# Kernel tuning notes

Hardware: AMD Instinct MI355X
Metric: run time of the kernel (lower is better)

The kernel has to match this reference:

```python
import jax, jax.numpy as jnp
import numpy as np


def _elem_mlp(x, w1, b1, w2, b2):
    # elementwise 1 -> N -> 1 ReLU MLP (distilled exp / inv approximators)
    h = jax.nn.relu(x[..., None] * w1[:, 0] + b1)  # [..., N]
    return jnp.einsum('...n,n->...', h, w2[0]) + b2[0]


def setup_inputs() -> dict:
    key = jax.random.key(0)
    ks = jax.random.split(key, 13)
    T, S, B, D = 8, 512, 8, 512
    NE, NI = 32, 64
    f = jnp.float32
    inp = {
        'sx': jax.random.normal(ks[0], (T, S, B, D), f) * 0.1,
        'q_proj_weight': jax.random.normal(ks[1], (D, D), f) / np.sqrt(D),
        'k_proj_weight': jax.random.normal(ks[2], (D, D), f) / np.sqrt(D),
        'q_proj_bias': jax.random.normal(ks[3], (D,), f) * 0.02,
        'k_proj_bias': jax.random.normal(ks[4], (D,), f) * 0.02,
        'exp_w1': jax.random.normal(ks[5], (NE, 1), f),
        'exp_b1': jax.random.normal(ks[6], (NE,), f) * 0.1,
        'exp_w2': jax.random.normal(ks[7], (1, NE), f) / np.sqrt(NE),
        'exp_b2': jax.random.normal(ks[8], (1,), f) * 0.01,
        'inv_w1': jax.random.normal(ks[9], (NI, 1), f),
        'inv_b1': jax.random.normal(ks[10], (NI,), f) * 0.1,
        'inv_w2': jax.random.normal(ks[11], (1, NI), f) / np.sqrt(NI),
        'inv_b2': jax.random.normal(ks[12], (1,), f) * 0.01,
        'num_heads': 8,
    }
    return inp


def reference(sx, q_proj_weight, k_proj_weight, q_proj_bias, k_proj_bias,
              exp_w1, exp_b1, exp_w2, exp_b2,
              inv_w1, inv_b1, inv_w2, inv_b2, num_heads):
    T, S, B, D = sx.shape
    H = num_heads
    hd = D // H
    scale = 1.0 / np.sqrt(hd)

    def proj(x_t, W, b):
        # [S, B, D] -> [B*H, S, hd]
        y = x_t @ W.T + b
        return y.reshape(S, B * H, hd).transpose(1, 0, 2)

    def step(carry, x_t):
        sum_q, sum_k, sum_p = carry
        sq = proj(x_t, q_proj_weight, q_proj_bias)
        sk = proj(x_t, k_proj_weight, k_proj_bias)
        sum_q = sum_q + sq
        # sp_t = sum_q @ sk^T + sq @ sum_k^T (sum_k updated AFTER, per snn_qk_product)
        sp = (jnp.einsum('bsh,bth->bst', sum_q, sk)
              + jnp.einsum('bsh,bth->bst', sq, sum_k)) * scale
        sum_k = sum_k + sk
        return (sum_q, sum_k, sum_p + sp), None

    z_qk = jnp.zeros((B * H, S, hd), sx.dtype)
    z_p = jnp.zeros((B * H, S, S), sx.dtype)
    (sum_q, sum_k, sum_p), _ = jax.lax.scan(step, (z_qk, z_qk, z_p), sx)

    p = sum_p / T  # time-averaged accumulated QK product

    # fit_softmax: distilled-MLP softmax approximation
    tmax = p[:, :, 0:1]
    tp = jnp.minimum(p - (tmax - 1.0), 3.0)
    x_up = jnp.where(tp > -20.0,
                     _elem_mlp(tp, exp_w1, exp_b1, exp_w2, exp_b2), 0.0)
    partition = x_up.sum(-1, keepdims=True)
    p_inv = _elem_mlp(partition, inv_w1, inv_b1, inv_w2, inv_b2)
    out = x_up * p_inv
    partition_p2 = out.sum(-1, keepdims=True)
    p_inv2 = _elem_mlp(partition_p2, inv_w1, inv_b1, inv_w2, inv_b2)
    out2 = jnp.where(partition_p2 > 1.5, out * p_inv2, out)
    return out2
```

## Files before the change

### kernel.cpp

```cpp
#include <hip/hip_runtime.h>


#define T_  8
#define NE_ 32
#define NI_ 64

#define LUT_N   4096
#define LUT_LO  -20.0f
#define LUT_HI  3.0f
#define LUT_INVW (LUT_N / (LUT_HI - LUT_LO))
#define LUT_W    ((LUT_HI - LUT_LO) / LUT_N)

typedef __attribute__((ext_vector_type(8))) short bf16x8;
typedef __attribute__((ext_vector_type(4))) float f32x4;

#define XS_OFF 0u
#define WQ_OFF 2097152u
#define WK_OFF 2359296u
#define QB_OFF 2621440u
#define KB_OFF 4718592u
#define LUT_OFF 6815744u

__device__ inline unsigned short f2bf(float f) {
  union { float f; unsigned u; } v; v.f = f;
  unsigned r = v.u + 0x7FFFu + ((v.u >> 16) & 1u);
  return (unsigned short)(r >> 16);
}

__device__ inline void gload16(const void* g, void* l) {
  __builtin_amdgcn_global_load_lds(
      (const __attribute__((address_space(1))) void*)g,
      (__attribute__((address_space(3))) void*)l, 16, 0, 0);
}

__device__ inline bf16x8 lds_read_swz(const unsigned short* base, int row, int byteoff) {
  int addr = row * 128 + (byteoff ^ ((row & 7) << 4));
  return *(const bf16x8*)((const char*)base + addr);
}

__device__ inline float invmlp(float x, const float* __restrict__ w1,
                               const float* __restrict__ b1,
                               const float* __restrict__ w2, float b2) {
  float a = b2;
  for (int n = 0; n < NI_; n++) a += w2[n] * fmaxf(x * w1[n] + b1[n], 0.0f);
  return a;
}

__device__ inline float expmlp_exact(float t, const float* __restrict__ w1,
                                     const float* __restrict__ b1,
                                     const float* __restrict__ w2, float b2) {
  float a = b2;
#pragma unroll
  for (int n = 0; n < NE_; n++) a += w2[n] * fmaxf(t * w1[n] + b1[n], 0.0f);
  return a;
}

__global__ __launch_bounds__(256) void k_pre(
    const float* __restrict__ sx, const float* __restrict__ wq,
    const float* __restrict__ wk, const float* __restrict__ ew1,
    const float* __restrict__ eb1, const float* __restrict__ ew2,
    const float* __restrict__ eb2p,
    unsigned short* __restrict__ xs, unsigned short* __restrict__ wqb,
    unsigned short* __restrict__ wkb, float2* __restrict__ lut) {
  int bx = blockIdx.x, tid = threadIdx.x;
  if (bx < 2048) {
    size_t i = ((size_t)bx * 256 + tid) * 4;
    float4 a = *(const float4*)(sx + i);
#pragma unroll
    for (int t = 1; t < T_; t++) {
      float4 v = *(const float4*)(sx + (size_t)t * 2097152 + i);
      a.x += v.x; a.y += v.y; a.z += v.z; a.w += v.w;
    }
    ushort4 o; o.x = f2bf(a.x); o.y = f2bf(a.y); o.z = f2bf(a.z); o.w = f2bf(a.w);
    *(ushort4*)(xs + i) = o;
  } else if (bx < 2560) {
    const float* src = (bx < 2304) ? wq : wk;
    unsigned short* dst = (bx < 2304) ? wqb : wkb;
    int base = (bx < 2304) ? 2048 : 2304;
    size_t i = ((size_t)(bx - base) * 256 + tid) * 4;
    float4 a = *(const float4*)(src + i);
    ushort4 o; o.x = f2bf(a.x); o.y = f2bf(a.y); o.z = f2bf(a.z); o.w = f2bf(a.w);
    *(ushort4*)(dst + i) = o;
  } else {
    int i = (bx - 2560) * 256 + tid;
    float b2 = eb2p[0];
    float tl = fmaf((float)i, LUT_W, LUT_LO);
    float th = fmaf((float)(i + 1), LUT_W, LUT_LO);
    float el = expmlp_exact(tl, ew1, eb1, ew2, b2);
    float eh = expmlp_exact(th, ew1, eb1, ew2, b2);
    float alpha = (eh - el) * LUT_INVW;
    float beta = fmaf(-alpha, tl, el);
    lut[i] = make_float2(alpha, beta);
  }
}

__global__ __launch_bounds__(256, 2) void k_proj(
    const unsigned short* __restrict__ xs, const unsigned short* __restrict__ wb,
    const float* __restrict__ bq, const float* __restrict__ bk,
    unsigned short* __restrict__ outb) {
  __shared__ unsigned short As[128 * 64];
  __shared__ unsigned short Bs[128 * 64];
  int tid = threadIdx.x;
  int lane = tid & 63, w = tid >> 6;
  int r0 = blockIdx.x * 128;
  int c0 = blockIdx.y * 128;
  int z = blockIdx.z;
  const unsigned short* W = wb + (size_t)z * 262144;
  const float* bias = z ? bk : bq;
  unsigned short* dst = outb + (size_t)z * 2097152;
  float sc = z ? 1.0f : (1.0f / 64.0f);

  int rgrp = lane >> 4, cl = lane & 15;
  int r0w = (w >> 1) * 64, c0w = (w & 1) * 64;

  f32x4 acc[4][4];
  f32x4 zero = {0.f, 0.f, 0.f, 0.f};
#pragma unroll
  for (int m = 0; m < 4; m++)
#pragma unroll
    for (int n = 0; n < 4; n++) acc[m][n] = zero;

  int rl = lane >> 3, slot = lane & 7;

  for (int kt = 0; kt < 8; kt++) {
    int k0 = kt * 64;
#pragma unroll
    for (int i = 0; i < 4; i++) {
      int chunk = w * 4 + i;
      int r = chunk * 8 + rl;
      int sw = (slot ^ (r & 7)) * 8;
      gload16(xs + (size_t)(r0 + r) * 512 + k0 + sw, (char*)As + chunk * 1024);
      gload16(W + (size_t)(c0 + r) * 512 + k0 + sw, (char*)Bs + chunk * 1024);
    }
    __syncthreads();
#pragma unroll
    for (int kb = 0; kb < 2; kb++) {
      bf16x8 af[4], bfr[4];
#pragma unroll
      for (int m = 0; m < 4; m++) af[m] = lds_read_swz(As, r0w + 16 * m + cl, kb * 64 + rgrp * 16);
#pragma unroll
      for (int n = 0; n < 4; n++) bfr[n] = lds_read_swz(Bs, c0w + 16 * n + cl, kb * 64 + rgrp * 16);
#pragma unroll
      for (int m = 0; m < 4; m++)
#pragma unroll
        for (int n = 0; n < 4; n++)
          acc[m][n] = __builtin_amdgcn_mfma_f32_16x16x32_bf16(af[m], bfr[n], acc[m][n], 0, 0, 0);
    }
    __syncthreads();
  }

#pragma unroll
  for (int n = 0; n < 4; n++) {
    int cg = c0 + c0w + 16 * n + cl;
    float bv = 8.0f * bias[cg];
    int h = cg >> 6, dh = cg & 63;
#pragma unroll
    for (int m = 0; m < 4; m++) {
#pragma unroll
      for (int j = 0; j < 4; j++) {
        int rg = r0 + r0w + 16 * m + rgrp * 4 + j;
        int s = rg >> 3, b = rg & 7;
        dst[((size_t)(b * 8 + h) * 512 + s) * 64 + dh] = f2bf((acc[m][n][j] + bv) * sc);
      }
    }
  }
}

__global__ __launch_bounds__(512, 4) void k_attn(
    const unsigned short* __restrict__ qb, const unsigned short* __restrict__ kb,
    const float2* __restrict__ lutg,
    const float* __restrict__ iw1, const float* __restrict__ ib1,
    const float* __restrict__ iw2, const float* __restrict__ ib2p,
    float* __restrict__ out) {
  __shared__ float2 Lut[LUT_N];
  __shared__ float s_tmax[32];
  __shared__ float s_part[4][32];
  __shared__ float s_fac[32];

  int tid = threadIdx.x;
  int lane = tid & 63, w = tid >> 6;
  int rt = blockIdx.x, bh = blockIdx.y;
  int rs = w & 1, ch = w >> 1;
  int r0 = rt * 32;
  int c0 = ch * 128;
  int rgrp = lane >> 4, cl = lane & 15;

#pragma unroll
  for (int i = 0; i < 4; i++) {
    int chunk = w * 4 + i;
    gload16((const char*)lutg + chunk * 1024 + lane * 16, (char*)Lut + chunk * 1024);
  }

  const unsigned short* Kg = kb + (size_t)bh * (512 * 64);
  const unsigned short* Qg = qb + (size_t)bh * (512 * 64);

  const bf16x8* qrow = (const bf16x8*)(Qg + (size_t)(r0 + rs * 16 + cl) * 64);
  bf16x8 aF0 = qrow[rgrp];
  bf16x8 aF1 = qrow[4 + rgrp];

  f32x4 acc[8];
  f32x4 zero = {0.f, 0.f, 0.f, 0.f};
#pragma unroll
  for (int f = 0; f < 8; f++) {
    const bf16x8* krow = (const bf16x8*)(Kg + (size_t)(c0 + 16 * f + cl) * 64);
    bf16x8 b0 = krow[rgrp];
    bf16x8 b1 = krow[4 + rgrp];
    acc[f] = __builtin_amdgcn_mfma_f32_16x16x32_bf16(aF0, b0, zero, 0, 0, 0);
    acc[f] = __builtin_amdgcn_mfma_f32_16x16x32_bf16(aF1, b1, acc[f], 0, 0, 0);
  }

  if (ch == 0 && cl == 0) {
#pragma unroll
    for (int j = 0; j < 4; j++) s_tmax[rs * 16 + rgrp * 4 + j] = acc[0][j] - 1.0f;
  }
  __syncthreads();

  float tm1[4];
#pragma unroll
  for (int j = 0; j < 4; j++) tm1[j] = s_tmax[rs * 16 + rgrp * 4 + j];

  const float C0 = -LUT_LO * LUT_INVW;
  float rowsum[4] = {0.f, 0.f, 0.f, 0.f};
#pragma unroll
  for (int f = 0; f < 8; f++) {
#pragma unroll
    for (int j = 0; j < 4; j++) {
      float tp = fminf(acc[f][j] - tm1[j], 3.0f);
      float u = fmaf(tp, LUT_INVW, C0);
      u = fminf(fmaxf(u, 0.0f), (float)(LUT_N - 1));
      float2 ab = Lut[(int)u];
      float xu = fmaf(ab.x, tp, ab.y);
      xu = (tp > -20.0f) ? xu : 0.0f;
      acc[f][j] = xu;
      rowsum[j] += xu;
    }
  }

#pragma unroll
  for (int j = 0; j < 4; j++) {
    float s = rowsum[j];
    s += __shfl_xor(s, 1);
    s += __shfl_xor(s, 2);
    s += __shfl_xor(s, 4);
    s += __shfl_xor(s, 8);
    if (cl == 0) s_part[ch][rs * 16 + rgrp * 4 + j] = s;
  }
  __syncthreads();

  if (tid < 32) {
    float part = s_part[0][tid] + s_part[1][tid] + s_part[2][tid] + s_part[3][tid];
    float pinv = invmlp(part, iw1, ib1, iw2, ib2p[0]);
    float pp2 = part * pinv;
    float fac = pinv;
    if (pp2 > 1.5f) fac *= invmlp(pp2, iw1, ib1, iw2, ib2p[0]);
    s_fac[tid] = fac;
  }
  __syncthreads();

  float* outb = out + ((size_t)bh * 512 + r0) * 512;
#pragma unroll
  for (int j = 0; j < 4; j++) {
    int row = rs * 16 + rgrp * 4 + j;
    float fac = s_fac[row];
#pragma unroll
    for (int f = 0; f < 8; f++)
      outb[(size_t)row * 512 + c0 + 16 * f + cl] = acc[f][j] * fac;
  }
}

extern "C" void kernel_launch(void* const* d_in, const int* in_sizes, int n_in,
                              void* d_out, int out_size, void* d_ws, size_t ws_size,
                              hipStream_t stream) {
  (void)in_sizes; (void)n_in; (void)out_size; (void)ws_size;
  const float* sx  = (const float*)d_in[0];
  const float* wq  = (const float*)d_in[1];
  const float* wk  = (const float*)d_in[2];
  const float* bq  = (const float*)d_in[3];
  const float* bk  = (const float*)d_in[4];
  const float* ew1 = (const float*)d_in[5];
  const float* eb1 = (const float*)d_in[6];
  const float* ew2 = (const float*)d_in[7];
  const float* eb2 = (const float*)d_in[8];
  const float* iw1 = (const float*)d_in[9];
  const float* ib1 = (const float*)d_in[10];
  const float* iw2 = (const float*)d_in[11];
  const float* ib2 = (const float*)d_in[12];
  unsigned short* wsu = (unsigned short*)d_ws;
  float2* lut = (float2*)(wsu + LUT_OFF);
  float* out = (float*)d_out;

  k_pre<<<2576, 256, 0, stream>>>(sx, wq, wk, ew1, eb1, ew2, eb2,
                                  wsu + XS_OFF, wsu + WQ_OFF, wsu + WK_OFF, lut);
  k_proj<<<dim3(32, 4, 2), 256, 0, stream>>>(wsu + XS_OFF, wsu + WQ_OFF, bq, bk, wsu + QB_OFF);
  k_attn<<<dim3(16, 64), 512, 0, stream>>>(wsu + QB_OFF, wsu + KB_OFF, lut,
                                           iw1, ib1, iw2, ib2, out);
}
```

Measured before the change: 60.76 us.

## Pack Q/K in MFMA fragment layout and enlarge attention tiles with XCD-aware mapping

The projection kernel now writes Q and K in a fragment-packed layout, so each lane of the attention kernel loads its bf16x8 operand from one contiguous 16-byte slot. Before, each lane gathered strided pieces of 64-element rows. Each attention block now covers 64 rows by all 512 columns, with 16 accumulator fragments per wave. This halves the block count and the number of LUT copies loaded into LDS. Block indices are remapped so that blocks sharing a batch-head land on the same XCD for L2 reuse. The cost is higher register pressure from 16 live accumulators per wave, which may reduce occupancy.

```diff
diff --git a/kernel.cpp b/kernel.cpp
--- a/kernel.cpp
+++ b/kernel.cpp
@@ -154,13 +154,17 @@
     int cg = c0 + c0w + 16 * n + cl;
     float bv = 8.0f * bias[cg];
     int h = cg >> 6, dh = cg & 63;
+    int chunk = dh >> 3, hh = chunk >> 2, rg2 = chunk & 3, jj = dh & 7;
 #pragma unroll
     for (int m = 0; m < 4; m++) {
 #pragma unroll
       for (int j = 0; j < 4; j++) {
         int rg = r0 + r0w + 16 * m + rgrp * 4 + j;
         int s = rg >> 3, b = rg & 7;
-        dst[((size_t)(b * 8 + h) * 512 + s) * 64 + dh] = f2bf((acc[m][n][j] + bv) * sc);
+        int bh = b * 8 + h;
+        int cb = s >> 4, cls = s & 15;
+        size_t idx = ((size_t)((bh * 32 + cb) * 2 + hh)) * 512 + (rg2 * 16 + cls) * 8 + jj;
+        dst[idx] = f2bf((acc[m][n][j] + bv) * sc);
       }
     }
   }
@@ -173,38 +177,38 @@
     const float* __restrict__ iw2, const float* __restrict__ ib2p,
     float* __restrict__ out) {
   __shared__ float2 Lut[LUT_N];
-  __shared__ float s_tmax[32];
-  __shared__ float s_part[4][32];
-  __shared__ float s_fac[32];
+  __shared__ float s_tmax[64];
+  __shared__ float s_part[2][64];
+  __shared__ float s_fac[64];
 
   int tid = threadIdx.x;
   int lane = tid & 63, w = tid >> 6;
-  int rt = blockIdx.x, bh = blockIdx.y;
-  int rs = w & 1, ch = w >> 1;
-  int r0 = rt * 32;
-  int c0 = ch * 128;
+  int i = blockIdx.x;
+  int xcd = i & 7, j2 = i >> 3;
+  int bh = xcd * 8 + (j2 >> 3);
+  int rt = j2 & 7;
+  int ch = w & 1, rs = w >> 1;
   int rgrp = lane >> 4, cl = lane & 15;
 
 #pragma unroll
-  for (int i = 0; i < 4; i++) {
-    int chunk = w * 4 + i;
+  for (int c = 0; c < 4; c++) {
+    int chunk = w * 4 + c;
     gload16((const char*)lutg + chunk * 1024 + lane * 16, (char*)Lut + chunk * 1024);
   }
 
-  const unsigned short* Kg = kb + (size_t)bh * (512 * 64);
-  const unsigned short* Qg = qb + (size_t)bh * (512 * 64);
-
-  const bf16x8* qrow = (const bf16x8*)(Qg + (size_t)(r0 + rs * 16 + cl) * 64);
-  bf16x8 aF0 = qrow[rgrp];
-  bf16x8 aF1 = qrow[4 + rgrp];
-
-  f32x4 acc[8];
+  int rb = rt * 4 + rs;
+  const char* Qb = (const char*)qb + (size_t)((bh * 32 + rb) * 2) * 1024;
+  bf16x8 aF0 = *(const bf16x8*)(Qb + lane * 16);
+  bf16x8 aF1 = *(const bf16x8*)(Qb + 1024 + lane * 16);
+
+  f32x4 acc[16];
   f32x4 zero = {0.f, 0.f, 0.f, 0.f};
 #pragma unroll
-  for (int f = 0; f < 8; f++) {
-    const bf16x8* krow = (const bf16x8*)(Kg + (size_t)(c0 + 16 * f + cl) * 64);
-    bf16x8 b0 = krow[rgrp];
-    bf16x8 b1 = krow[4 + rgrp];
+  for (int f = 0; f < 16; f++) {
+    int cb = ch * 16 + f;
+    const char* Kb = (const char*)kb + (size_t)((bh * 32 + cb) * 2) * 1024;
+    bf16x8 b0 = *(const bf16x8*)(Kb + lane * 16);
+    bf16x8 b1 = *(const bf16x8*)(Kb + 1024 + lane * 16);
     acc[f] = __builtin_amdgcn_mfma_f32_16x16x32_bf16(aF0, b0, zero, 0, 0, 0);
     acc[f] = __builtin_amdgcn_mfma_f32_16x16x32_bf16(aF1, b1, acc[f], 0, 0, 0);
   }
@@ -222,7 +226,7 @@
   const float C0 = -LUT_LO * LUT_INVW;
   float rowsum[4] = {0.f, 0.f, 0.f, 0.f};
 #pragma unroll
-  for (int f = 0; f < 8; f++) {
+  for (int f = 0; f < 16; f++) {
 #pragma unroll
     for (int j = 0; j < 4; j++) {
       float tp = fminf(acc[f][j] - tm1[j], 3.0f);
@@ -247,8 +251,8 @@
   }
   __syncthreads();
 
-  if (tid < 32) {
-    float part = s_part[0][tid] + s_part[1][tid] + s_part[2][tid] + s_part[3][tid];
+  if (tid < 64) {
+    float part = s_part[0][tid] + s_part[1][tid];
     float pinv = invmlp(part, iw1, ib1, iw2, ib2p[0]);
     float pp2 = part * pinv;
     float fac = pinv;
@@ -257,14 +261,14 @@
   }
   __syncthreads();
 
-  float* outb = out + ((size_t)bh * 512 + r0) * 512;
+  float* outb = out + ((size_t)bh * 512 + rt * 64) * 512;
 #pragma unroll
   for (int j = 0; j < 4; j++) {
     int row = rs * 16 + rgrp * 4 + j;
     float fac = s_fac[row];
 #pragma unroll
-    for (int f = 0; f < 8; f++)
-      outb[(size_t)row * 512 + c0 + 16 * f + cl] = acc[f][j] * fac;
+    for (int f = 0; f < 16; f++)
+      outb[(size_t)row * 512 + ch * 256 + 16 * f + cl] = acc[f][j] * fac;
   }
 }
 
@@ -292,6 +296,6 @@
   k_pre<<<2576, 256, 0, stream>>>(sx, wq, wk, ew1, eb1, ew2, eb2,
                                   wsu + XS_OFF, wsu + WQ_OFF, wsu + WK_OFF, lut);
   k_proj<<<dim3(32, 4, 2), 256, 0, stream>>>(wsu + XS_OFF, wsu + WQ_OFF, bq, bk, wsu + QB_OFF);
-  k_attn<<<dim3(16, 64), 512, 0, stream>>>(wsu + QB_OFF, wsu + KB_OFF, lut,
-                                           iw1, ib1, iw2, ib2, out);
-}
+  k_attn<<<512, 512, 0, stream>>>(wsu + QB_OFF, wsu + KB_OFF, lut,
+                                  iw1, ib1, iw2, ib2, out);
+}
```

Measured after the change: 64.27 us. 1.06x slower.
